# Kernel optimization log

Measured on AMD Instinct MI355X. Metric: run time of the kernel, lower is better.

Reference implementation:

```python
import jax, jax.numpy as jnp
import numpy as np

NEG_INF = -1.0e9  # matches torch code's masked fill value


def setup_inputs() -> dict:
    key = jax.random.key(0)
    k1, k2, k3, k4 = jax.random.split(key, 4)
    n, q, s, d, v = 8, 4096, 4096, 64, 64
    return {
        "queries_nqd": jax.random.normal(k1, (n, q, d), dtype=jnp.float32),
        "keys_nsd": jax.random.normal(k2, (n, s, d), dtype=jnp.float32),
        "values_nsv": jax.random.normal(k3, (n, s, v), dtype=jnp.float32),
        "attention_mask_nqs": jax.random.randint(k4, (n, q, s), 0, 2).astype(jnp.bool_),
    }


def reference(queries_nqd, keys_nsd, values_nsv, attention_mask_nqs):
    d = queries_nqd.shape[-1]
    scale = 1.0 / jnp.sqrt(jnp.asarray(d, dtype=queries_nqd.dtype))
    # [n,q,s] = [n,q,d] @ [n,d,s]
    scores_nqs = jnp.einsum("nqd,nsd->nqs", queries_nqd, keys_nsd) * scale
    scores_nqs = jnp.where(attention_mask_nqs, scores_nqs, jnp.asarray(NEG_INF, scores_nqs.dtype))
    probs_nqs = jax.nn.softmax(scores_nqs, axis=-1)
    # dropout p=0.0 (eval) -> identity
    return jnp.einsum("nqs,nsv->nqv", probs_nqs, values_nsv)
```

## Files before the change

kernel.cpp:

```cpp
#include <hip/hip_runtime.h>
#include <hip/hip_bf16.h>


#define NHEADS 8
#define QLEN   4096
#define SLEN   4096
#define DDIM   64
#define VDIM   64
#define PBLK   128
#define QBLK   128
#define NPHASE (SLEN / PBLK)

typedef __bf16          bf16x4 __attribute__((ext_vector_type(4)));
typedef __bf16          bf16x8 __attribute__((ext_vector_type(8)));
typedef float           f32x4  __attribute__((ext_vector_type(4)));
typedef float           f32x16 __attribute__((ext_vector_type(16)));
typedef unsigned int    u32x4  __attribute__((ext_vector_type(4)));
typedef unsigned short  u16x4  __attribute__((ext_vector_type(4)));

#define KSWZ(s) (((s) & 7) << 4)
#define VSWZ(v) ((((v) >> 2) & 7) << 4)
#define CLAMPP(p) ((p) < NPHASE ? (p) : NPHASE - 1)

#define LDS_BARRIER() do {                                          \
  asm volatile("s_waitcnt lgkmcnt(0)" ::: "memory");                \
  __builtin_amdgcn_s_barrier();                                     \
  __builtin_amdgcn_sched_barrier(0);                                \
} while (0)

__device__ __forceinline__ f32x16 zero16() {
  f32x16 z;
#pragma unroll
  for (int i = 0; i < 16; ++i) z[i] = 0.f;
  return z;
}

__device__ __forceinline__ unsigned short bfb(float x) {
  return __builtin_bit_cast(unsigned short, (__bf16)x);
}
__device__ __forceinline__ unsigned pk2(float a, float b) {
  return (unsigned)bfb(a) | ((unsigned)bfb(b) << 16);
}

__device__ __forceinline__ int detect_mfmt(const unsigned char* __restrict__ M) {
  const int lane = threadIdx.x & 63;
  u32x4 w = *((const u32x4*)M + lane);
  unsigned o = w[0] | w[1] | w[2] | w[3];
  unsigned comb = ((o & 0x00FFFF00u) ? 1u : 0u) | ((o & 0x000000FFu) ? 2u : 0u);
  comb |= __shfl_xor((int)comb, 1);  comb |= __shfl_xor((int)comb, 2);
  comb |= __shfl_xor((int)comb, 4);  comb |= __shfl_xor((int)comb, 8);
  comb |= __shfl_xor((int)comb, 16); comb |= __shfl_xor((int)comb, 32);
  return ((comb & 1u) == 0u) ? 1 : (((comb & 2u) == 0u) ? 2 : 0);
}

template<bool U8>
__global__ __launch_bounds__(512, 2)
void attn_fwd(const float* __restrict__ Qg, const float* __restrict__ Kg,
              const float* __restrict__ Vg, const unsigned char* __restrict__ Mg,
              float* __restrict__ Og)
{
  __shared__ __align__(16) unsigned short Ksh[2][128 * 64];
  __shared__ __align__(16) unsigned short Vsh[2][64 * 128];

  {
    const int mfmt = detect_mfmt(Mg);
    if (U8 ? (mfmt != 0) : (mfmt == 0)) return;
  }

  const int tid   = threadIdx.x;
  const int wave  = tid >> 6;
  const int lane  = tid & 63;
  const int qtile = wave & 3;
  const int shalf = wave >> 2;
  const int lq    = lane & 31;
  const int h     = lane >> 5;

  const int head = blockIdx.x;
  const int qblk = blockIdx.y;

  const float* Qp = Qg + ((size_t)head * QLEN + (size_t)qblk * QBLK) * DDIM;
  const float* Kp = Kg + (size_t)head * SLEN * DDIM;
  const float* Vp = Vg + (size_t)head * SLEN * VDIM;
  float* Op = Og + ((size_t)head * QLEN + (size_t)qblk * QBLK) * DDIM;

  const float QSCALE = 0.125f * 1.44269504f;
  const int qrow = qtile * 32 + lq;
  bf16x8 qf[4];
#pragma unroll
  for (int kd = 0; kd < 4; ++kd) {
    const float* qp = Qp + (size_t)qrow * DDIM + 16 * kd + 8 * h;
    f32x4 a = *(const f32x4*)qp;
    f32x4 b = *(const f32x4*)(qp + 4);
    bf16x8 t;
#pragma unroll
    for (int j = 0; j < 4; ++j) { t[j] = (__bf16)(a[j] * QSCALE); t[4 + j] = (__bf16)(b[j] * QSCALE); }
    qf[kd] = t;
  }

  const size_t mbase = ((size_t)head * QLEN + (size_t)qblk * QBLK + qrow) * SLEN;
  const unsigned char* mrow8  = Mg + mbase;
  const unsigned*      mrow32 = (const unsigned*)Mg + mbase;

  f32x16 oacc[2];
  oacc[0] = zero16(); oacc[1] = zero16();
  float m_run = -INFINITY;
  float l_run = 0.f;

  f32x4 kp0, kp1, kp2, kp3, vp0, vp1, vp2, vp3;
  unsigned m8A[8],  m8B[8];
  u32x4    m32A[8], m32B[8];

#define PREFETCH_KV(P)                                                         \
  {                                                                            \
    size_t b_ = (size_t)CLAMPP(P) * PBLK;                                      \
    int sr_ = tid >> 4, d0_ = (tid & 15) * 4;                                  \
    kp0 = *(const f32x4*)(Kp + (b_ + sr_     ) * DDIM + d0_);                  \
    kp1 = *(const f32x4*)(Kp + (b_ + sr_ + 32) * DDIM + d0_);                  \
    kp2 = *(const f32x4*)(Kp + (b_ + sr_ + 64) * DDIM + d0_);                  \
    kp3 = *(const f32x4*)(Kp + (b_ + sr_ + 96) * DDIM + d0_);                  \
    vp0 = *(const f32x4*)(Vp + (b_ + sr_     ) * VDIM + d0_);                  \
    vp1 = *(const f32x4*)(Vp + (b_ + sr_ + 32) * VDIM + d0_);                  \
    vp2 = *(const f32x4*)(Vp + (b_ + sr_ + 64) * VDIM + d0_);                  \
    vp3 = *(const f32x4*)(Vp + (b_ + sr_ + 96) * VDIM + d0_);                  \
  }

#define WRITE_ONE(BUF, KP, VP, IT)                                             \
  {                                                                            \
    int srow = (tid >> 4) + (IT) * 32;                                         \
    int d0   = (tid & 15) * 4;                                                 \
    bf16x4 kb;                                                                 \
    _Pragma("unroll") for (int j = 0; j < 4; ++j) kb[j] = (__bf16)KP[j];       \
    int koff = (srow * 128 + d0 * 2) ^ KSWZ(srow);                             \
    *(u16x4*)((char*)Ksh[BUF] + koff) = __builtin_bit_cast(u16x4, kb);         \
    _Pragma("unroll")                                                          \
    for (int j = 0; j < 4; ++j) {                                              \
      int v = d0 + j;                                                          \
      unsigned short b = __builtin_bit_cast(unsigned short, (__bf16)VP[j]);    \
      int voff = (v * 256 + srow * 2) ^ VSWZ(v);                               \
      *(unsigned short*)((char*)Vsh[BUF] + voff) = b;                          \
    }                                                                          \
  }

#define WRITE_KV(BUF)                                                          \
  WRITE_ONE(BUF, kp0, vp0, 0) WRITE_ONE(BUF, kp1, vp1, 1)                      \
  WRITE_ONE(BUF, kp2, vp2, 2) WRITE_ONE(BUF, kp3, vp3, 3)

#define LOAD_MASK(M8, M32, P)                                                  \
  if constexpr (U8) {                                                          \
    _Pragma("unroll")                                                          \
    for (int st2 = 0; st2 < 2; ++st2)                                          \
      _Pragma("unroll")                                                        \
      for (int st = 0; st < 4; ++st)                                           \
        M8[4 * st2 + st] = *(const unsigned*)(mrow8 + (size_t)CLAMPP(P) * PBLK \
                           + 64 * shalf + 32 * st2 + 8 * st + 4 * h);          \
  } else {                                                                     \
    _Pragma("unroll")                                                          \
    for (int st2 = 0; st2 < 2; ++st2)                                          \
      _Pragma("unroll")                                                        \
      for (int st = 0; st < 4; ++st)                                           \
        M32[4 * st2 + st] = *(const u32x4*)(mrow32 + (size_t)CLAMPP(P) * PBLK  \
                           + 64 * shalf + 32 * st2 + 8 * st + 4 * h);          \
  }

#define TILE(CUR, ST2, MU8, MU32) {                                            \
                       \
  f32x16 sacc = zero16();                                                      \
  int srow_ = 64 * shalf + 32 * (ST2) + lq;                                    \
  __builtin_amdgcn_s_setprio(1);                                               \
  _Pragma("unroll")                                                            \
  for (int kd = 0; kd < 4; ++kd) {                                             \
    int off = (srow_ * 128 + (32 * kd + 16 * h)) ^ KSWZ(srow_);                \
    bf16x8 kf = *(const bf16x8*)((const char*)Ksh[CUR] + off);                 \
    sacc = __builtin_amdgcn_mfma_f32_32x32x16_bf16(kf, qf[kd], sacc, 0, 0, 0); \
  }                                                                            \
  __builtin_amdgcn_s_setprio(0);                                               \
                     \
  float vals[4][4];                                                            \
  float mloc = -INFINITY;                                                      \
  _Pragma("unroll")                                                            \
  for (int st = 0; st < 4; ++st) {                                             \
    bool keep[4];                                                              \
    if constexpr (U8) {                                                        \
      unsigned w_ = MU8[4 * (ST2) + st];                                       \
      _Pragma("unroll")                                                        \
      for (int r = 0; r < 4; ++r) keep[r] = ((w_ >> (8 * r)) & 0xFFu) != 0u;   \
    } else {                                                                   \
      _Pragma("unroll")                                                        \
      for (int r = 0; r < 4; ++r) keep[r] = MU32[4 * (ST2) + st][r] != 0u;     \
    }                                                                          \
    _Pragma("unroll")                                                          \
    for (int r = 0; r < 4; ++r) {                                              \
      float v = keep[r] ? sacc[4 * st + r] : -1.0e9f;                          \
      vals[st][r] = v;                                                         \
      mloc = fmaxf(mloc, v);                                                   \
    }                                                                          \
  }                                                                            \
  mloc = fmaxf(mloc, __shfl_xor(mloc, 32));                                    \
  if (!__all(mloc <= m_run + 8.0f)) {                   \
    float m_new = fmaxf(m_run, mloc);                                          \
    float alpha = __builtin_amdgcn_exp2f(m_run - m_new);                       \
    l_run *= alpha;                                                            \
    _Pragma("unroll")                                                          \
    for (int vt = 0; vt < 2; ++vt)                                             \
      _Pragma("unroll")                                                        \
      for (int r = 0; r < 16; ++r) oacc[vt][r] *= alpha;                       \
    m_run = m_new;                                                             \
  }                                                                            \
                 \
  float lsum = 0.f;                                                            \
  unsigned wlo[4], whi[4];                                                     \
  _Pragma("unroll")                                                            \
  for (int st = 0; st < 4; ++st) {                                             \
    float p0 = __builtin_amdgcn_exp2f(vals[st][0] - m_run);                    \
    float p1 = __builtin_amdgcn_exp2f(vals[st][1] - m_run);                    \
    float p2 = __builtin_amdgcn_exp2f(vals[st][2] - m_run);                    \
    float p3 = __builtin_amdgcn_exp2f(vals[st][3] - m_run);                    \
    lsum += (p0 + p1) + (p2 + p3);                                             \
    wlo[st] = pk2(p0, p1);                                                     \
    whi[st] = pk2(p2, p3);                                                     \
  }                                                                            \
  lsum += __shfl_xor(lsum, 32);                                                \
  l_run += lsum;                                                               \
   \
   \
   \
  _Pragma("unroll")                                                            \
  for (int ks2 = 0; ks2 < 2; ++ks2) {                                          \
    unsigned slo = h ? wlo[2 * ks2] : wlo[2 * ks2 + 1];    \
    unsigned shi = h ? whi[2 * ks2] : whi[2 * ks2 + 1];                        \
    unsigned rlo = __shfl_xor(slo, 32);                                        \
    unsigned rhi = __shfl_xor(shi, 32);                                        \
    unsigned klo = h ? wlo[2 * ks2 + 1] : wlo[2 * ks2];    \
    unsigned khi = h ? whi[2 * ks2 + 1] : whi[2 * ks2];                        \
    u32x4 fw;                                                                  \
    fw[0] = h ? rlo : klo;  fw[1] = h ? rhi : khi;                             \
    fw[2] = h ? klo : rlo;  fw[3] = h ? khi : rhi;                             \
    bf16x8 pf = __builtin_bit_cast(bf16x8, fw);                                \
    __builtin_amdgcn_s_setprio(1);                                             \
    _Pragma("unroll")                                                          \
    for (int vt = 0; vt < 2; ++vt) {                                           \
      int vrow = 32 * vt + lq;                                                 \
      int voff = (vrow * 256 + (128 * shalf + 64 * (ST2) + 32 * ks2 + 16 * h)) \
                 ^ VSWZ(vrow);                                                 \
      bf16x8 vf = *(const bf16x8*)((const char*)Vsh[CUR] + voff);              \
      oacc[vt] = __builtin_amdgcn_mfma_f32_32x32x16_bf16(vf, pf, oacc[vt], 0, 0, 0); \
    }                                                                          \
    __builtin_amdgcn_s_setprio(0);                                             \
  }                                                                            \
}

#define PHASE_BODY(P, CUR, MU8, MU32, ML8, ML32) {                             \
  PREFETCH_KV((P) + 1);                                                        \
  LOAD_MASK(ML8, ML32, (P) + 1);                                               \
  TILE(CUR, 0, MU8, MU32);                                                     \
  TILE(CUR, 1, MU8, MU32);                                                     \
  WRITE_KV((CUR) ^ 1);                                                         \
  LDS_BARRIER();                                                               \
}

  PREFETCH_KV(0);
  LOAD_MASK(m8A, m32A, 0);
  WRITE_KV(0);
  LDS_BARRIER();

  for (int pp = 0; pp < NPHASE; pp += 2) {
    PHASE_BODY(pp,     0, m8A, m32A, m8B, m32B);
    PHASE_BODY(pp + 1, 1, m8B, m32B, m8A, m32A);
  }

  float* mO = (float*)&Ksh[0][0];
  float* mM = (float*)&Vsh[0][0];
  if (shalf == 1) {
#pragma unroll
    for (int vt = 0; vt < 2; ++vt) {
#pragma unroll
      for (int st = 0; st < 4; ++st) {
#pragma unroll
        for (int r = 0; r < 4; ++r) {
          int v = 32 * vt + 8 * st + 4 * h + r;
          mO[((size_t)qtile * 64 + v) * 32 + lq] = oacc[vt][4 * st + r];
        }
      }
    }
    if (h == 0) {
      mM[(qtile * 2 + 0) * 32 + lq] = m_run;
      mM[(qtile * 2 + 1) * 32 + lq] = l_run;
    }
  }
  LDS_BARRIER();
  if (shalf == 0) {
    float m1 = mM[(qtile * 2 + 0) * 32 + lq];
    float l1 = mM[(qtile * 2 + 1) * 32 + lq];
    float mm = fmaxf(m_run, m1);
    float a0 = __builtin_amdgcn_exp2f(m_run - mm);
    float a1 = __builtin_amdgcn_exp2f(m1 - mm);
    float inv = 1.0f / (l_run * a0 + l1 * a1);
    float* orow = Op + (size_t)qrow * VDIM;
#pragma unroll
    for (int vt = 0; vt < 2; ++vt) {
#pragma unroll
      for (int st = 0; st < 4; ++st) {
        int v0 = 32 * vt + 8 * st + 4 * h;
        f32x4 o;
#pragma unroll
        for (int r = 0; r < 4; ++r) {
          float o1 = mO[((size_t)qtile * 64 + v0 + r) * 32 + lq];
          o[r] = (oacc[vt][4 * st + r] * a0 + o1 * a1) * inv;
        }
        *(f32x4*)(orow + v0) = o;
      }
    }
  }
#undef PREFETCH_KV
#undef WRITE_ONE
#undef WRITE_KV
#undef LOAD_MASK
#undef TILE
#undef PHASE_BODY
}

extern "C" void kernel_launch(void* const* d_in, const int* in_sizes, int n_in,
                              void* d_out, int out_size, void* d_ws, size_t ws_size,
                              hipStream_t stream) {
  const float* Qg = (const float*)d_in[0];
  const float* Kg = (const float*)d_in[1];
  const float* Vg = (const float*)d_in[2];
  const unsigned char* Mg = (const unsigned char*)d_in[3];
  float* Og = (float*)d_out;

  dim3 grid(NHEADS, QLEN / QBLK);
  dim3 block(512);
  attn_fwd<true ><<<grid, block, 0, stream>>>(Qg, Kg, Vg, Mg, Og);
  attn_fwd<false><<<grid, block, 0, stream>>>(Qg, Kg, Vg, Mg, Og);
}
```

Before: 158.2 us.

## Split key blocks across four wave groups with 1024-thread blocks

The block grows from 512 to 1024 threads. Each of four wave groups now processes one 32-key slice of every 128-key phase, where before two groups each handled 64 keys. That halves per-wave work per phase and the mask and K/V prefetch registers, and the staging loads become 8-wide. The partial softmax states are merged in a two-level LDS reduction with extra barriers. The aim is more waves in flight to hide latency of mask streaming, at the cost of more barrier and merge overhead and a 64KB LDS footprint that may limit blocks per CU.

```diff
diff --git a/kernel.cpp b/kernel.cpp
--- a/kernel.cpp
+++ b/kernel.cpp
@@ -11,12 +11,10 @@
 #define QBLK   128
 #define NPHASE (SLEN / PBLK)
 
-typedef __bf16          bf16x4 __attribute__((ext_vector_type(4)));
 typedef __bf16          bf16x8 __attribute__((ext_vector_type(8)));
 typedef float           f32x4  __attribute__((ext_vector_type(4)));
 typedef float           f32x16 __attribute__((ext_vector_type(16)));
 typedef unsigned int    u32x4  __attribute__((ext_vector_type(4)));
-typedef unsigned short  u16x4  __attribute__((ext_vector_type(4)));
 
 #define KSWZ(s) (((s) & 7) << 4)
 #define VSWZ(v) ((((v) >> 2) & 7) << 4)
@@ -34,7 +32,6 @@
   for (int i = 0; i < 16; ++i) z[i] = 0.f;
   return z;
 }
-
 __device__ __forceinline__ unsigned short bfb(float x) {
   return __builtin_bit_cast(unsigned short, (__bf16)x);
 }
@@ -54,13 +51,13 @@
 }
 
 template<bool U8>
-__global__ __launch_bounds__(512, 2)
+__global__ __launch_bounds__(1024, 4)
 void attn_fwd(const float* __restrict__ Qg, const float* __restrict__ Kg,
               const float* __restrict__ Vg, const unsigned char* __restrict__ Mg,
               float* __restrict__ Og)
 {
-  __shared__ __align__(16) unsigned short Ksh[2][128 * 64];
-  __shared__ __align__(16) unsigned short Vsh[2][64 * 128];
+  __shared__ __align__(16) unsigned char LB[65536];
+  __shared__ float mM[2][4][2][32];
 
   {
     const int mfmt = detect_mfmt(Mg);
@@ -71,7 +68,7 @@
   const int wave  = tid >> 6;
   const int lane  = tid & 63;
   const int qtile = wave & 3;
-  const int shalf = wave >> 2;
+  const int sq    = wave >> 2;
   const int lq    = lane & 31;
   const int h     = lane >> 5;
 
@@ -82,6 +79,11 @@
   const float* Kp = Kg + (size_t)head * SLEN * DDIM;
   const float* Vp = Vg + (size_t)head * SLEN * VDIM;
   float* Op = Og + ((size_t)head * QLEN + (size_t)qblk * QBLK) * DDIM;
+
+  char* const Kb0 = (char*)LB;
+  char* const Kb1 = (char*)LB + 16384;
+  char* const Vb0 = (char*)LB + 32768;
+  char* const Vb1 = (char*)LB + 49152;
 
   const float QSCALE = 0.125f * 1.44269504f;
   const int qrow = qtile * 32 + lq;
@@ -97,7 +99,8 @@
     qf[kd] = t;
   }
 
-  const size_t mbase = ((size_t)head * QLEN + (size_t)qblk * QBLK + qrow) * SLEN;
+  const size_t mbase = ((size_t)head * QLEN + (size_t)qblk * QBLK + qrow) * SLEN
+                     + (size_t)sq * 32;
   const unsigned char* mrow8  = Mg + mbase;
   const unsigned*      mrow32 = (const unsigned*)Mg + mbase;
 
@@ -106,87 +109,71 @@
   float m_run = -INFINITY;
   float l_run = 0.f;
 
-  f32x4 kp0, kp1, kp2, kp3, vp0, vp1, vp2, vp3;
-  unsigned m8A[8],  m8B[8];
-  u32x4    m32A[8], m32B[8];
+  f32x4 kpr0, kpr1, vpr0, vpr1;
+  unsigned m8A[4],  m8B[4];
+  u32x4    m32A[4], m32B[4];
 
 #define PREFETCH_KV(P)                                                         \
   {                                                                            \
     size_t b_ = (size_t)CLAMPP(P) * PBLK;                                      \
-    int sr_ = tid >> 4, d0_ = (tid & 15) * 4;                                  \
-    kp0 = *(const f32x4*)(Kp + (b_ + sr_     ) * DDIM + d0_);                  \
-    kp1 = *(const f32x4*)(Kp + (b_ + sr_ + 32) * DDIM + d0_);                  \
-    kp2 = *(const f32x4*)(Kp + (b_ + sr_ + 64) * DDIM + d0_);                  \
-    kp3 = *(const f32x4*)(Kp + (b_ + sr_ + 96) * DDIM + d0_);                  \
-    vp0 = *(const f32x4*)(Vp + (b_ + sr_     ) * VDIM + d0_);                  \
-    vp1 = *(const f32x4*)(Vp + (b_ + sr_ + 32) * VDIM + d0_);                  \
-    vp2 = *(const f32x4*)(Vp + (b_ + sr_ + 64) * VDIM + d0_);                  \
-    vp3 = *(const f32x4*)(Vp + (b_ + sr_ + 96) * VDIM + d0_);                  \
-  }
-
-#define WRITE_ONE(BUF, KP, VP, IT)                                             \
+    int sr_ = tid >> 3, d0_ = (tid & 7) * 8;                                   \
+    kpr0 = *(const f32x4*)(Kp + (b_ + sr_) * DDIM + d0_);                      \
+    kpr1 = *(const f32x4*)(Kp + (b_ + sr_) * DDIM + d0_ + 4);                  \
+    vpr0 = *(const f32x4*)(Vp + (b_ + sr_) * VDIM + d0_);                      \
+    vpr1 = *(const f32x4*)(Vp + (b_ + sr_) * VDIM + d0_ + 4);                  \
+  }
+
+#define WRITE_KV(KB, VB)                                                       \
   {                                                                            \
-    int srow = (tid >> 4) + (IT) * 32;                                         \
-    int d0   = (tid & 15) * 4;                                                 \
-    bf16x4 kb;                                                                 \
-    _Pragma("unroll") for (int j = 0; j < 4; ++j) kb[j] = (__bf16)KP[j];       \
+    int srow = tid >> 3, d0 = (tid & 7) * 8;                                   \
+    bf16x8 kb;                                                                 \
+    _Pragma("unroll")                                                          \
+    for (int j = 0; j < 4; ++j) { kb[j] = (__bf16)kpr0[j]; kb[4 + j] = (__bf16)kpr1[j]; } \
     int koff = (srow * 128 + d0 * 2) ^ KSWZ(srow);                             \
-    *(u16x4*)((char*)Ksh[BUF] + koff) = __builtin_bit_cast(u16x4, kb);         \
-    _Pragma("unroll")                                                          \
-    for (int j = 0; j < 4; ++j) {                                              \
+    *(bf16x8*)((KB) + koff) = kb;                                              \
+    _Pragma("unroll")                                                          \
+    for (int j = 0; j < 8; ++j) {                                              \
       int v = d0 + j;                                                          \
-      unsigned short b = __builtin_bit_cast(unsigned short, (__bf16)VP[j]);    \
+      float x = (j < 4) ? vpr0[j] : vpr1[j - 4];                               \
       int voff = (v * 256 + srow * 2) ^ VSWZ(v);                               \
-      *(unsigned short*)((char*)Vsh[BUF] + voff) = b;                          \
-    }                                                                          \
-  }
-
-#define WRITE_KV(BUF)                                                          \
-  WRITE_ONE(BUF, kp0, vp0, 0) WRITE_ONE(BUF, kp1, vp1, 1)                      \
-  WRITE_ONE(BUF, kp2, vp2, 2) WRITE_ONE(BUF, kp3, vp3, 3)
+      *(unsigned short*)((VB) + voff) = bfb(x);                                \
+    }                                                                          \
+  }
 
 #define LOAD_MASK(M8, M32, P)                                                  \
   if constexpr (U8) {                                                          \
     _Pragma("unroll")                                                          \
-    for (int st2 = 0; st2 < 2; ++st2)                                          \
-      _Pragma("unroll")                                                        \
-      for (int st = 0; st < 4; ++st)                                           \
-        M8[4 * st2 + st] = *(const unsigned*)(mrow8 + (size_t)CLAMPP(P) * PBLK \
-                           + 64 * shalf + 32 * st2 + 8 * st + 4 * h);          \
+    for (int st = 0; st < 4; ++st)                                             \
+      M8[st] = *(const unsigned*)(mrow8 + (size_t)CLAMPP(P) * PBLK + 8 * st + 4 * h); \
   } else {                                                                     \
     _Pragma("unroll")                                                          \
-    for (int st2 = 0; st2 < 2; ++st2)                                          \
-      _Pragma("unroll")                                                        \
-      for (int st = 0; st < 4; ++st)                                           \
-        M32[4 * st2 + st] = *(const u32x4*)(mrow32 + (size_t)CLAMPP(P) * PBLK  \
-                           + 64 * shalf + 32 * st2 + 8 * st + 4 * h);          \
-  }
-
-#define TILE(CUR, ST2, MU8, MU32) {                                            \
-                       \
+    for (int st = 0; st < 4; ++st)                                             \
+      M32[st] = *(const u32x4*)(mrow32 + (size_t)CLAMPP(P) * PBLK + 8 * st + 4 * h); \
+  }
+
+#define TILE(KB, VB, MU8, MU32) {                                              \
   f32x16 sacc = zero16();                                                      \
-  int srow_ = 64 * shalf + 32 * (ST2) + lq;                                    \
+  int srow_ = sq * 32 + lq;                                                    \
   __builtin_amdgcn_s_setprio(1);                                               \
   _Pragma("unroll")                                                            \
   for (int kd = 0; kd < 4; ++kd) {                                             \
     int off = (srow_ * 128 + (32 * kd + 16 * h)) ^ KSWZ(srow_);                \
-    bf16x8 kf = *(const bf16x8*)((const char*)Ksh[CUR] + off);                 \
+    bf16x8 kf = *(const bf16x8*)((KB) + off);                                  \
     sacc = __builtin_amdgcn_mfma_f32_32x32x16_bf16(kf, qf[kd], sacc, 0, 0, 0); \
   }                                                                            \
   __builtin_amdgcn_s_setprio(0);                                               \
-                     \
   float vals[4][4];                                                            \
   float mloc = -INFINITY;                                                      \
   _Pragma("unroll")                                                            \
   for (int st = 0; st < 4; ++st) {                                             \
     bool keep[4];                                                              \
     if constexpr (U8) {                                                        \
-      unsigned w_ = MU8[4 * (ST2) + st];                                       \
+      unsigned w_ = MU8[st];                                                   \
       _Pragma("unroll")                                                        \
       for (int r = 0; r < 4; ++r) keep[r] = ((w_ >> (8 * r)) & 0xFFu) != 0u;   \
     } else {                                                                   \
       _Pragma("unroll")                                                        \
-      for (int r = 0; r < 4; ++r) keep[r] = MU32[4 * (ST2) + st][r] != 0u;     \
+      for (int r = 0; r < 4; ++r) keep[r] = MU32[st][r] != 0u;                 \
     }                                                                          \
     _Pragma("unroll")                                                          \
     for (int r = 0; r < 4; ++r) {                                              \
@@ -206,7 +193,6 @@
       for (int r = 0; r < 16; ++r) oacc[vt][r] *= alpha;                       \
     m_run = m_new;                                                             \
   }                                                                            \
-                 \
   float lsum = 0.f;                                                            \
   unsigned wlo[4], whi[4];                                                     \
   _Pragma("unroll")                                                            \
@@ -222,15 +208,13 @@
   lsum += __shfl_xor(lsum, 32);                                                \
   l_run += lsum;                                                               \
    \
-   \
-   \
   _Pragma("unroll")                                                            \
   for (int ks2 = 0; ks2 < 2; ++ks2) {                                          \
-    unsigned slo = h ? wlo[2 * ks2] : wlo[2 * ks2 + 1];    \
+    unsigned slo = h ? wlo[2 * ks2] : wlo[2 * ks2 + 1];                        \
     unsigned shi = h ? whi[2 * ks2] : whi[2 * ks2 + 1];                        \
     unsigned rlo = __shfl_xor(slo, 32);                                        \
     unsigned rhi = __shfl_xor(shi, 32);                                        \
-    unsigned klo = h ? wlo[2 * ks2 + 1] : wlo[2 * ks2];    \
+    unsigned klo = h ? wlo[2 * ks2 + 1] : wlo[2 * ks2];                        \
     unsigned khi = h ? whi[2 * ks2 + 1] : whi[2 * ks2];                        \
     u32x4 fw;                                                                  \
     fw[0] = h ? rlo : klo;  fw[1] = h ? rhi : khi;                             \
@@ -240,61 +224,80 @@
     _Pragma("unroll")                                                          \
     for (int vt = 0; vt < 2; ++vt) {                                           \
       int vrow = 32 * vt + lq;                                                 \
-      int voff = (vrow * 256 + (128 * shalf + 64 * (ST2) + 32 * ks2 + 16 * h)) \
-                 ^ VSWZ(vrow);                                                 \
-      bf16x8 vf = *(const bf16x8*)((const char*)Vsh[CUR] + voff);              \
+      int voff = (vrow * 256 + (64 * sq + 32 * ks2 + 16 * h)) ^ VSWZ(vrow);    \
+      bf16x8 vf = *(const bf16x8*)((VB) + voff);                               \
       oacc[vt] = __builtin_amdgcn_mfma_f32_32x32x16_bf16(vf, pf, oacc[vt], 0, 0, 0); \
     }                                                                          \
     __builtin_amdgcn_s_setprio(0);                                             \
   }                                                                            \
 }
 
-#define PHASE_BODY(P, CUR, MU8, MU32, ML8, ML32) {                             \
+#define PHASE_BODY(P, KBc, VBc, KBn, VBn, MU8, MU32, ML8, ML32) {              \
   PREFETCH_KV((P) + 1);                                                        \
   LOAD_MASK(ML8, ML32, (P) + 1);                                               \
-  TILE(CUR, 0, MU8, MU32);                                                     \
-  TILE(CUR, 1, MU8, MU32);                                                     \
-  WRITE_KV((CUR) ^ 1);                                                         \
+  TILE(KBc, VBc, MU8, MU32);                                                   \
+  WRITE_KV(KBn, VBn);                                                          \
   LDS_BARRIER();                                                               \
 }
 
   PREFETCH_KV(0);
   LOAD_MASK(m8A, m32A, 0);
-  WRITE_KV(0);
+  WRITE_KV(Kb0, Vb0);
   LDS_BARRIER();
 
   for (int pp = 0; pp < NPHASE; pp += 2) {
-    PHASE_BODY(pp,     0, m8A, m32A, m8B, m32B);
-    PHASE_BODY(pp + 1, 1, m8B, m32B, m8A, m32A);
-  }
-
-  float* mO = (float*)&Ksh[0][0];
-  float* mM = (float*)&Vsh[0][0];
-  if (shalf == 1) {
-#pragma unroll
-    for (int vt = 0; vt < 2; ++vt) {
-#pragma unroll
-      for (int st = 0; st < 4; ++st) {
-#pragma unroll
-        for (int r = 0; r < 4; ++r) {
-          int v = 32 * vt + 8 * st + 4 * h + r;
-          mO[((size_t)qtile * 64 + v) * 32 + lq] = oacc[vt][4 * st + r];
-        }
-      }
-    }
-    if (h == 0) {
-      mM[(qtile * 2 + 0) * 32 + lq] = m_run;
-      mM[(qtile * 2 + 1) * 32 + lq] = l_run;
-    }
-  }
+    PHASE_BODY(pp,     Kb0, Vb0, Kb1, Vb1, m8A, m32A, m8B, m32B);
+    PHASE_BODY(pp + 1, Kb1, Vb1, Kb0, Vb0, m8B, m32B, m8A, m32A);
+  }
+
+#define PUBLISH(SLOT) {                                                        \
+    float* mOs = (float*)LB + (SLOT) * 8192;                                   \
+    _Pragma("unroll")                                                          \
+    for (int vt = 0; vt < 2; ++vt)                                             \
+      _Pragma("unroll")                                                        \
+      for (int st = 0; st < 4; ++st)                                           \
+        _Pragma("unroll")                                                      \
+        for (int r = 0; r < 4; ++r) {                                          \
+          int v = 32 * vt + 8 * st + 4 * h + r;                                \
+          mOs[((size_t)qtile * 64 + v) * 32 + lq] = oacc[vt][4 * st + r];      \
+        }                                                                      \
+    if (h == 0) {                                                              \
+      mM[SLOT][qtile][0][lq] = m_run;                                          \
+      mM[SLOT][qtile][1][lq] = l_run;                                          \
+    }                                                                          \
+  }
+#define MERGE(SLOT) {                                                          \
+    float m1 = mM[SLOT][qtile][0][lq];                                         \
+    float l1 = mM[SLOT][qtile][1][lq];                                         \
+    float mm = fmaxf(m_run, m1);                                               \
+    float a0 = __builtin_amdgcn_exp2f(m_run - mm);                             \
+    float a1 = __builtin_amdgcn_exp2f(m1 - mm);                                \
+    m_run = mm;                                                                \
+    l_run = l_run * a0 + l1 * a1;                                              \
+    const float* mOs = (const float*)LB + (SLOT) * 8192;                       \
+    _Pragma("unroll")                                                          \
+    for (int vt = 0; vt < 2; ++vt)                                             \
+      _Pragma("unroll")                                                        \
+      for (int st = 0; st < 4; ++st)                                           \
+        _Pragma("unroll")                                                      \
+        for (int r = 0; r < 4; ++r) {                                          \
+          int v = 32 * vt + 8 * st + 4 * h + r;                                \
+          float o1 = mOs[((size_t)qtile * 64 + v) * 32 + lq];                  \
+          oacc[vt][4 * st + r] = oacc[vt][4 * st + r] * a0 + o1 * a1;          \
+        }                                                                      \
+  }
+
+  if (sq == 1) PUBLISH(0);
+  if (sq == 3) PUBLISH(1);
   LDS_BARRIER();
-  if (shalf == 0) {
-    float m1 = mM[(qtile * 2 + 0) * 32 + lq];
-    float l1 = mM[(qtile * 2 + 1) * 32 + lq];
-    float mm = fmaxf(m_run, m1);
-    float a0 = __builtin_amdgcn_exp2f(m_run - mm);
-    float a1 = __builtin_amdgcn_exp2f(m1 - mm);
-    float inv = 1.0f / (l_run * a0 + l1 * a1);
+  if (sq == 0) MERGE(0);
+  if (sq == 2) MERGE(1);
+  LDS_BARRIER();
+  if (sq == 2) PUBLISH(0);
+  LDS_BARRIER();
+  if (sq == 0) {
+    MERGE(0);
+    float inv_l = 1.0f / l_run;
     float* orow = Op + (size_t)qrow * VDIM;
 #pragma unroll
     for (int vt = 0; vt < 2; ++vt) {
@@ -303,20 +306,18 @@
         int v0 = 32 * vt + 8 * st + 4 * h;
         f32x4 o;
 #pragma unroll
-        for (int r = 0; r < 4; ++r) {
-          float o1 = mO[((size_t)qtile * 64 + v0 + r) * 32 + lq];
-          o[r] = (oacc[vt][4 * st + r] * a0 + o1 * a1) * inv;
-        }
+        for (int r = 0; r < 4; ++r) o[r] = oacc[vt][4 * st + r] * inv_l;
         *(f32x4*)(orow + v0) = o;
       }
     }
   }
 #undef PREFETCH_KV
-#undef WRITE_ONE
 #undef WRITE_KV
 #undef LOAD_MASK
 #undef TILE
 #undef PHASE_BODY
+#undef PUBLISH
+#undef MERGE
 }
 
 extern "C" void kernel_launch(void* const* d_in, const int* in_sizes, int n_in,
@@ -329,7 +330,7 @@
   float* Og = (float*)d_out;
 
   dim3 grid(NHEADS, QLEN / QBLK);
-  dim3 block(512);
+  dim3 block(1024);
   attn_fwd<true ><<<grid, block, 0, stream>>>(Qg, Kg, Vg, Mg, Og);
   attn_fwd<false><<<grid, block, 0, stream>>>(Qg, Kg, Vg, Mg, Og);
 }
```

Result: slower. 337.0 us (+113.1%).
